# Kernel tuning notes

Hardware: AMD Instinct MI355X
Metric: run time of the kernel (lower is better)

Reference implementation:

```python
import jax, jax.numpy as jnp
import numpy as np

EPS = 1e-12  # F.normalize eps


def _l2norm(v):
    n = jnp.sqrt(jnp.sum(v * v, axis=-1, keepdims=True))
    return v / jnp.maximum(n, EPS)


def setup_inputs() -> dict:
    key = jax.random.key(0)
    ks = jax.random.split(key, 6)
    B, S, D, F, E = 2, 2048, 1024, 4096, 8
    std = 0.02
    return {
        "x": jax.random.normal(ks[0], (B, S, D), jnp.float32),
        "Wp": jax.random.normal(ks[1], (D, D), jnp.float32) * (1.0 / np.sqrt(D)),
        "sim_matrix": jax.random.normal(ks[2], (E, D), jnp.float32) * std,
        "temperature": jnp.asarray(1.0, jnp.float32),
        "W1": jax.random.normal(ks[3], (E, D, F), jnp.float32) * (1.0 / np.sqrt(D)),
        "b1": jnp.zeros((E, F), jnp.float32),
        "W2": jax.random.normal(ks[4], (E, F, D), jnp.float32) * (1.0 / np.sqrt(F)),
        "b2": jnp.zeros((E, D), jnp.float32),
    }


def reference(x, Wp, sim_matrix, temperature, W1, b1, W2, b2):
    # ---- cosine gate ----
    E = sim_matrix.shape[0]
    top_k = 2
    proj = jnp.einsum("bsd,ed->bse", x, Wp)            # Linear(d,d), weight [out,in]
    pn = _l2norm(proj)                                   # [B,S,D]
    sn = _l2norm(sim_matrix)                             # [E,D]
    gate_scores = jnp.einsum("bsd,ed->bse", pn, sn) / temperature
    top_v, top_i = jax.lax.top_k(gate_scores, top_k)     # [B,S,K]
    gate_probs = jax.nn.softmax(top_v, axis=-1)          # [B,S,K]
    # per-token combine weight per expert: sum_k prob_k * 1[idx_k==e]
    comb = jnp.sum(jax.nn.one_hot(top_i, E, dtype=x.dtype) * gate_probs[..., None], axis=-2)  # [B,S,E]
    # ---- experts (dense over all experts, masked combine = original math) ----
    h = jax.nn.gelu(jnp.einsum("bsd,edf->ebsf", x, W1) + b1[:, None, None, :], approximate=False)
    eo = jnp.einsum("ebsf,efd->ebsd", h, W2) + b2[:, None, None, :]  # [E,B,S,D]
    out = jnp.einsum("ebsd,bse->bsd", eo, comb)
    return out
```

## Files before the change

kernel.cpp:

```cpp
#include <hip/hip_runtime.h>
#include <hip/hip_bf16.h>
#include <math.h>

#define NTOK 4096
#define DD 1024
#define FF 4096
#define NEXP 8
#define EBM 128
#define EBN 128
#define EBK 32
#define PAIR_CAP 9216
#define TILES_MAX 72

typedef short bf16x8 __attribute__((ext_vector_type(8)));
typedef float f32x4 __attribute__((ext_vector_type(4)));
typedef unsigned short u16x8 __attribute__((ext_vector_type(8)));

__device__ __forceinline__ ushort f2bf(float x) {
  unsigned u = __float_as_uint(x);
  unsigned r = (u + 0x7FFFu + ((u >> 16) & 1u)) >> 16;
  return (ushort)r;
}

__device__ __forceinline__ void async16(const void* g, void* l) {
  __builtin_amdgcn_global_load_lds(
      (const __attribute__((address_space(1))) char*)g,
      (__attribute__((address_space(3))) char*)l, 16, 0, 0);
}


__global__ void k_convert4(const float4* __restrict__ s, ushort* __restrict__ d, int n4) {
  int i = blockIdx.x * 256 + threadIdx.x;
  if (i >= n4) return;
  float4 v = s[i];
  ushort4 o;
  o.x = f2bf(v.x); o.y = f2bf(v.y); o.z = f2bf(v.z); o.w = f2bf(v.w);
  *(ushort4*)(d + (size_t)i * 4) = o;
}

__global__ void k_transpose(const float* __restrict__ src, ushort* __restrict__ dst,
                            int R, int C) {
  __shared__ float tile[128][65];
  int e = blockIdx.z;
  const float* s = src + (size_t)e * R * C;
  ushort* d = dst + (size_t)e * R * C;
  int c0 = blockIdx.x * 64, r0 = blockIdx.y * 128;
  int tid = threadIdx.x;
  int rr0 = tid >> 4;
  int cc4 = (tid & 15) * 4;
#pragma unroll
  for (int ps = 0; ps < 8; ++ps) {
    int r = ps * 16 + rr0;
    float4 v = *(const float4*)&s[(size_t)(r0 + r) * C + c0 + cc4];
    tile[r][cc4 + 0] = v.x; tile[r][cc4 + 1] = v.y;
    tile[r][cc4 + 2] = v.z; tile[r][cc4 + 3] = v.w;
  }
  __syncthreads();
  int cw = tid >> 4;
  int rp = (tid & 15) * 8;
#pragma unroll
  for (int pass = 0; pass < 4; ++pass) {
    int c = pass * 16 + cw;
    u16x8 o;
#pragma unroll
    for (int k = 0; k < 8; ++k) o[k] = f2bf(tile[rp + k][c]);
    *(u16x8*)&d[(size_t)(c0 + c) * R + r0 + rp] = o;
  }
}

__global__ void k_u(const float* __restrict__ wp, const float* __restrict__ sim,
                    double* __restrict__ u_part) {
  __shared__ double sred[256];
  int tid = threadIdx.x;
  int dblk = blockIdx.x, e = blockIdx.y, kc = blockIdx.z;
  double s = 0.0;
#pragma unroll
  for (int j = 0; j < 4; ++j) {
    double v = sim[e * DD + j * 256 + tid];
    s += v * v;
  }
  sred[tid] = s;
  __syncthreads();
  for (int m = 128; m; m >>= 1) {
    if (tid < m) sred[tid] += sred[tid + m];
    __syncthreads();
  }
  double sn = fmax(sqrt(sred[0]), 1e-12);
  int d = dblk * 256 + tid;
  int o0 = kc * 256;
  double acc = 0.0;
#pragma unroll 8
  for (int o = o0; o < o0 + 256; ++o)
    acc += (double)wp[(size_t)o * DD + d] * (double)sim[e * DD + o];
  u_part[((size_t)kc * NEXP + e) * DD + d] = acc / sn;
}

__global__ void k_ured(const double* __restrict__ up, double* __restrict__ u) {
  int i = blockIdx.x * 256 + threadIdx.x;
  u[i] = (up[i] + up[8192 + i]) + (up[16384 + i] + up[24576 + i]);
}

__global__ void k_gate(const float* __restrict__ x, const double* __restrict__ u,
                       const float* __restrict__ nu_part, const float* __restrict__ temp,
                       int* __restrict__ t2e, float* __restrict__ t2p) {
  int wid = threadIdx.x >> 6, lane = threadIdx.x & 63;
  int t = blockIdx.x * 4 + wid;
  double acc[NEXP];
#pragma unroll
  for (int e = 0; e < NEXP; ++e) acc[e] = 0.0;
  for (int d = lane; d < DD; d += 64) {
    double xv = x[(size_t)t * DD + d];
#pragma unroll
    for (int e = 0; e < NEXP; ++e) acc[e] += xv * u[e * DD + d];
  }
#pragma unroll
  for (int e = 0; e < NEXP; ++e)
    for (int m = 32; m; m >>= 1) acc[e] += __shfl_down(acc[e], m);
  float nv = (lane < 16) ? nu_part[t * 16 + lane] : 0.f;
  nv += __shfl_down(nv, 8); nv += __shfl_down(nv, 4);
  nv += __shfl_down(nv, 2); nv += __shfl_down(nv, 1);
  if (lane == 0) {
    double den = fmax(sqrt((double)nv), 1e-12) * (double)temp[0];
    double s[NEXP];
#pragma unroll
    for (int e = 0; e < NEXP; ++e) s[e] = acc[e] / den;
    int e1 = 0; double v1 = s[0];
    for (int e = 1; e < NEXP; ++e) if (s[e] > v1) { v1 = s[e]; e1 = e; }
    int e2 = -1; double v2 = -1e300;
    for (int e = 0; e < NEXP; ++e) if (e != e1 && s[e] > v2) { v2 = s[e]; e2 = e; }
    double z = exp(v2 - v1);
    double inv = 1.0 / (1.0 + z);
    t2e[t * 2] = e1; t2e[t * 2 + 1] = e2;
    t2p[t * 2] = (float)inv; t2p[t * 2 + 1] = (float)(z * inv);
  }
}

__global__ void k_count(const int* __restrict__ t2e, const float* __restrict__ t2p,
                        int* __restrict__ meta, int* __restrict__ ptok,
                        float* __restrict__ pp) {
  __shared__ int cnt[NEXP];
  int tid = threadIdx.x;
  for (int i = tid; i < PAIR_CAP; i += 256) { ptok[i] = 0; pp[i] = 0.f; }
  if (tid < NEXP) cnt[tid] = 0;
  __syncthreads();
  for (int i = tid; i < NTOK * 2; i += 256) atomicAdd(&cnt[t2e[i]], 1);
  __syncthreads();
  if (tid == 0) {
    int off = 0;
    for (int e = 0; e < NEXP; ++e) {
      meta[e] = cnt[e];
      meta[8 + e] = off;
      off += ((cnt[e] + EBM - 1) / EBM) * EBM;
    }
    meta[16] = off;
    meta[17] = off / EBM;
    for (int e = 0; e < NEXP; ++e) meta[18 + e] = 0;
    int ti = 0;
    for (int e = 0; e < NEXP; ++e) {
      int nt = (cnt[e] + EBM - 1) / EBM;
      for (int k = 0; k < nt; ++k) meta[26 + ti++] = e;
    }
  }
  __syncthreads();
  for (int i = tid; i < NTOK * 2; i += 256) {
    int e = t2e[i];
    int slot = atomicAdd(&meta[18 + e], 1);
    int pos = meta[8 + e] + slot;
    ptok[pos] = i >> 1;
    pp[pos] = t2p[i];
  }
}

template <int EPI>
__launch_bounds__(256, 4)
__global__ void gemm_x(const ushort* __restrict__ Abase, const ushort* __restrict__ Bbase,
                       int K, int Brows,
                       const int* __restrict__ pair_tok, const float* __restrict__ pair_p,
                       const int* __restrict__ meta, const float* __restrict__ bias,
                       float* __restrict__ nu_part, ushort* __restrict__ hout,
                       float* __restrict__ outp, int g_tiles, int nby, int tile0) {
  __shared__ ushort As[2][EBM * EBK];
  __shared__ ushort Bs[2][EBN * EBK];
  __shared__ int tok_s[EBM];
  __shared__ float p_s[EBM];

  const int tid = threadIdx.x;
  const int lane = tid & 63;
  const int wid = tid >> 6;

  int tile, nb;
  {
    int bid = blockIdx.x;
    if ((g_tiles & 1) == 0 && (nby & 3) == 0) {
      int x = bid & 7, b = bid >> 3;
      int i = x >> 2, j = x & 3;
      int nt = g_tiles >> 1, np = nby >> 2;
      int t_loc = b / np, p_loc = b - t_loc * np;
      tile = i * nt + t_loc;
      nb = j * np + p_loc;
    } else {
      tile = bid % g_tiles;
      nb = bid / g_tiles;
    }
  }
  tile += tile0;

  int expert = 0;
  if constexpr (EPI != 0) {
    if (tile >= meta[17]) return;
    expert = meta[26 + tile];
    if (tid < EBM) {
      int pr = tile * EBM + tid;
      tok_s[tid] = pair_tok[pr];
      p_s[tid] = pair_p[pr];
    }
    __syncthreads();
  }

  const char* Ac = (const char*)Abase;
  const char* Bc = (const char*)(Bbase + (size_t)expert * Brows * K);

  const char* asrc[2];
  const char* bsrc[2];
#pragma unroll
  for (int i = 0; i < 2; ++i) {
    int c = i * 256 + tid;
    int m = c >> 2, cc = c & 3;
    int sw = (cc ^ ((m >> 1) & 3)) << 4;
    int arow;
    if constexpr (EPI == 1) arow = tok_s[m];
    else if constexpr (EPI == 2) arow = (tile - tile0) * EBM + m;
    else arow = tile * EBM + m;
    asrc[i] = Ac + (size_t)arow * K * 2 + sw;
    bsrc[i] = Bc + (size_t)(nb * EBN + m) * K * 2 + sw;
  }

  const int wr = wid >> 1, wc = wid & 1;
  const int l15 = lane & 15, lg = lane >> 4;
  const int fxor = (l15 >> 1) & 3;

  f32x4 acc[4][4];
#pragma unroll
  for (int a = 0; a < 4; ++a)
#pragma unroll
    for (int b = 0; b < 4; ++b) acc[a][b] = (f32x4){0.f, 0.f, 0.f, 0.f};

  const int nk = K / EBK;

#pragma unroll
  for (int i = 0; i < 2; ++i) {
    async16(asrc[i], (char*)(&As[0][0]) + (i * 256 + wid * 64) * 16);
    async16(bsrc[i], (char*)(&Bs[0][0]) + (i * 256 + wid * 64) * 16);
  }

  for (int kt = 0; kt < nk; ++kt) {
    const int cur = kt & 1;
    __syncthreads();
    if (kt + 1 < nk) {
      const size_t ko = (size_t)(kt + 1) * EBK * 2;
#pragma unroll
      for (int i = 0; i < 2; ++i) {
        async16(asrc[i] + ko, (char*)(&As[cur ^ 1][0]) + (i * 256 + wid * 64) * 16);
        async16(bsrc[i] + ko, (char*)(&Bs[cur ^ 1][0]) + (i * 256 + wid * 64) * 16);
      }
    }
    const char* Ab = (const char*)(&As[cur][0]);
    const char* Bb = (const char*)(&Bs[cur][0]);
    bf16x8 af[4], bfr[4];
#pragma unroll
    for (int fi = 0; fi < 4; ++fi) {
      int r = wr * 64 + fi * 16 + l15;
      af[fi] = *(const bf16x8*)(Ab + r * 64 + (lg ^ fxor) * 16);
    }
#pragma unroll
    for (int fj = 0; fj < 4; ++fj) {
      int r = wc * 64 + fj * 16 + l15;
      bfr[fj] = *(const bf16x8*)(Bb + r * 64 + (lg ^ fxor) * 16);
    }
#pragma unroll
    for (int fi = 0; fi < 4; ++fi)
#pragma unroll
      for (int fj = 0; fj < 4; ++fj)
        acc[fi][fj] =
            __builtin_amdgcn_mfma_f32_16x16x32_bf16(af[fi], bfr[fj], acc[fi][fj], 0, 0, 0);
  }

  if constexpr (EPI == 0) {
#pragma unroll
    for (int fi = 0; fi < 4; ++fi) {
#pragma unroll
      for (int j = 0; j < 4; ++j) {
        float s = 0.f;
#pragma unroll
        for (int fj = 0; fj < 4; ++fj) { float v = acc[fi][fj][j]; s += v * v; }
        s += __shfl_xor(s, 1); s += __shfl_xor(s, 2);
        s += __shfl_xor(s, 4); s += __shfl_xor(s, 8);
        if (l15 == 0) {
          int row = tile * EBM + wr * 64 + fi * 16 + lg * 4 + j;
          nu_part[row * 16 + nb * 2 + wc] = s;
        }
      }
    }
  } else if constexpr (EPI == 1) {
    float bv[4];
#pragma unroll
    for (int fj = 0; fj < 4; ++fj)
      bv[fj] = bias[expert * FF + nb * EBN + wc * 64 + fj * 16 + l15];
#pragma unroll
    for (int fi = 0; fi < 4; ++fi)
#pragma unroll
      for (int fj = 0; fj < 4; ++fj)
#pragma unroll
        for (int j = 0; j < 4; ++j) {
          float v = acc[fi][fj][j] + bv[fj];
          float g = 0.5f * v * (1.0f + erff(v * 0.70710678118654752f));
          int rl = wr * 64 + fi * 16 + lg * 4 + j;
          size_t grow = (size_t)(tile - tile0) * EBM + rl;
          int col = nb * EBN + wc * 64 + fj * 16 + l15;
          hout[grow * FF + col] = f2bf(g);
        }
  } else {
    float bv[4];
#pragma unroll
    for (int fj = 0; fj < 4; ++fj)
      bv[fj] = bias[expert * DD + nb * EBN + wc * 64 + fj * 16 + l15];
#pragma unroll
    for (int fi = 0; fi < 4; ++fi) {
      int rl = wr * 64 + fi * 16 + lg * 4;
#pragma unroll
      for (int j = 0; j < 4; ++j) {
        int tok = tok_s[rl + j];
        float p = p_s[rl + j];
#pragma unroll
        for (int fj = 0; fj < 4; ++fj) {
          float v = (acc[fi][fj][j] + bv[fj]) * p;
          int col = nb * EBN + wc * 64 + fj * 16 + l15;
          atomicAdd(outp + (size_t)tok * DD + col, v);
        }
      }
    }
  }
}


extern "C" void kernel_launch(void* const* d_in, const int* in_sizes, int n_in,
                              void* d_out, int out_size, void* d_ws, size_t ws_size,
                              hipStream_t stream) {
  const float* x = (const float*)d_in[0];
  const float* wp = (const float*)d_in[1];
  const float* sim = (const float*)d_in[2];
  const float* temp = (const float*)d_in[3];
  const float* w1 = (const float*)d_in[4];
  const float* b1 = (const float*)d_in[5];
  const float* w2 = (const float*)d_in[6];
  const float* b2 = (const float*)d_in[7];
  float* out = (float*)d_out;

  char* w = (char*)d_ws;
  size_t off = 0;
  auto alloc = [&](size_t sz) {
    char* p = w + off;
    off = (off + sz + 255) & ~(size_t)255;
    return p;
  };
  double* u = (double*)alloc((size_t)NEXP * DD * 8);
  double* u_part = (double*)alloc((size_t)4 * NEXP * DD * 8);
  float* nu_part = (float*)alloc((size_t)NTOK * 16 * 4);
  int* t2e = (int*)alloc((size_t)NTOK * 2 * 4);
  float* t2p = (float*)alloc((size_t)NTOK * 2 * 4);
  int* meta = (int*)alloc(512);
  int* ptok = (int*)alloc((size_t)PAIR_CAP * 4);
  float* pp = (float*)alloc((size_t)PAIR_CAP * 4);
  ushort* xbf = (ushort*)alloc((size_t)NTOK * DD * 2);
  ushort* wpbf = (ushort*)alloc((size_t)DD * DD * 2);
  ushort* w1t = (ushort*)alloc((size_t)NEXP * DD * FF * 2);
  ushort* w2t = (ushort*)alloc((size_t)NEXP * DD * FF * 2);
  size_t havail = (ws_size > off) ? (ws_size - off) : 0;
  int G = (int)(havail / ((size_t)EBM * FF * 2));
  if (G > TILES_MAX) G = TILES_MAX;
  if (G >= 8) G &= ~7;
  if (G < 1) G = 1;
  ushort* h = (ushort*)(w + off);

  hipMemsetAsync(d_out, 0, (size_t)out_size * 4, stream);

  k_convert4<<<dim3(NTOK * DD / 4 / 256), 256, 0, stream>>>((const float4*)x, xbf, NTOK * DD / 4);
  k_convert4<<<dim3(DD * DD / 4 / 256), 256, 0, stream>>>((const float4*)wp, wpbf, DD * DD / 4);
  k_transpose<<<dim3(FF / 64, DD / 128, NEXP), 256, 0, stream>>>(w1, w1t, DD, FF);
  k_transpose<<<dim3(DD / 64, FF / 128, NEXP), 256, 0, stream>>>(w2, w2t, FF, DD);
  k_u<<<dim3(DD / 256, NEXP, 4), 256, 0, stream>>>(wp, sim, u_part);
  k_ured<<<dim3(NEXP * DD / 256), 256, 0, stream>>>(u_part, u);
  gemm_x<0><<<dim3((NTOK / EBM) * (DD / EBN)), 256, 0, stream>>>(
      xbf, wpbf, DD, DD, nullptr, nullptr, nullptr, nullptr, nu_part, nullptr, nullptr,
      NTOK / EBM, DD / EBN, 0);
  k_gate<<<dim3(NTOK / 4), 256, 0, stream>>>(x, u, nu_part, temp, t2e, t2p);
  k_count<<<1, 256, 0, stream>>>(t2e, t2p, meta, ptok, pp);

  for (int t0 = 0; t0 < TILES_MAX; t0 += G) {
    int g = TILES_MAX - t0;
    if (g > G) g = G;
    gemm_x<1><<<dim3(g * (FF / EBN)), 256, 0, stream>>>(
        xbf, w1t, DD, FF, ptok, pp, meta, b1, nullptr, h, nullptr, g, FF / EBN, t0);
    gemm_x<2><<<dim3(g * (DD / EBN)), 256, 0, stream>>>(
        h, w2t, FF, DD, ptok, pp, meta, b2, nullptr, nullptr, out, g, DD / EBN, t0);
  }
}
```

Before: 540.8 us.

## Split-K the second expert GEMM and parallelize pair scatter across blocks

The down-projection GEMM now launches with two K-chunks along blockIdx.y, and each chunk atomically adds its partial sum into the output, with the bias applied only by the first chunk. This doubles the block count for the small-N GEMM to fill more compute units. The token-to-expert scatter moves out of the single-block count kernel into a separate multi-block kernel. In exchange, the down-projection issues twice as many float atomics to the output and the scatter costs one more kernel launch.

```diff
diff --git a/kernel.cpp b/kernel.cpp
--- a/kernel.cpp
+++ b/kernel.cpp
@@ -135,9 +135,8 @@
   }
 }
 
-__global__ void k_count(const int* __restrict__ t2e, const float* __restrict__ t2p,
-                        int* __restrict__ meta, int* __restrict__ ptok,
-                        float* __restrict__ pp) {
+__global__ void k_count(const int* __restrict__ t2e, int* __restrict__ meta,
+                        int* __restrict__ ptok, float* __restrict__ pp) {
   __shared__ int cnt[NEXP];
   int tid = threadIdx.x;
   for (int i = tid; i < PAIR_CAP; i += 256) { ptok[i] = 0; pp[i] = 0.f; }
@@ -161,20 +160,24 @@
       for (int k = 0; k < nt; ++k) meta[26 + ti++] = e;
     }
   }
-  __syncthreads();
-  for (int i = tid; i < NTOK * 2; i += 256) {
-    int e = t2e[i];
-    int slot = atomicAdd(&meta[18 + e], 1);
-    int pos = meta[8 + e] + slot;
-    ptok[pos] = i >> 1;
-    pp[pos] = t2p[i];
-  }
+}
+
+__global__ void k_scatter(const int* __restrict__ t2e, const float* __restrict__ t2p,
+                          int* __restrict__ meta, int* __restrict__ ptok,
+                          float* __restrict__ pp) {
+  int i = blockIdx.x * 256 + threadIdx.x;
+  if (i >= NTOK * 2) return;
+  int e = t2e[i];
+  int slot = atomicAdd(&meta[18 + e], 1);
+  int pos = meta[8 + e] + slot;
+  ptok[pos] = i >> 1;
+  pp[pos] = t2p[i];
 }
 
 template <int EPI>
 __launch_bounds__(256, 4)
 __global__ void gemm_x(const ushort* __restrict__ Abase, const ushort* __restrict__ Bbase,
-                       int K, int Brows,
+                       int K, int Brows, int kchunk,
                        const int* __restrict__ pair_tok, const float* __restrict__ pair_p,
                        const int* __restrict__ meta, const float* __restrict__ bias,
                        float* __restrict__ nu_part, ushort* __restrict__ hout,
@@ -187,6 +190,7 @@
   const int tid = threadIdx.x;
   const int lane = tid & 63;
   const int wid = tid >> 6;
+  const int k0 = blockIdx.y * kchunk;
 
   int tile, nb;
   {
@@ -231,8 +235,8 @@
     if constexpr (EPI == 1) arow = tok_s[m];
     else if constexpr (EPI == 2) arow = (tile - tile0) * EBM + m;
     else arow = tile * EBM + m;
-    asrc[i] = Ac + (size_t)arow * K * 2 + sw;
-    bsrc[i] = Bc + (size_t)(nb * EBN + m) * K * 2 + sw;
+    asrc[i] = Ac + ((size_t)arow * K + k0) * 2 + sw;
+    bsrc[i] = Bc + ((size_t)(nb * EBN + m) * K + k0) * 2 + sw;
   }
 
   const int wr = wid >> 1, wc = wid & 1;
@@ -245,7 +249,7 @@
 #pragma unroll
     for (int b = 0; b < 4; ++b) acc[a][b] = (f32x4){0.f, 0.f, 0.f, 0.f};
 
-  const int nk = K / EBK;
+  const int nk = kchunk / EBK;
 
 #pragma unroll
   for (int i = 0; i < 2; ++i) {
@@ -321,9 +325,10 @@
         }
   } else {
     float bv[4];
+    const float bgate = (k0 == 0) ? 1.f : 0.f;
 #pragma unroll
     for (int fj = 0; fj < 4; ++fj)
-      bv[fj] = bias[expert * DD + nb * EBN + wc * 64 + fj * 16 + l15];
+      bv[fj] = bgate * bias[expert * DD + nb * EBN + wc * 64 + fj * 16 + l15];
 #pragma unroll
     for (int fi = 0; fi < 4; ++fi) {
       int rl = wr * 64 + fi * 16 + lg * 4;
@@ -391,17 +396,18 @@
   k_u<<<dim3(DD / 256, NEXP, 4), 256, 0, stream>>>(wp, sim, u_part);
   k_ured<<<dim3(NEXP * DD / 256), 256, 0, stream>>>(u_part, u);
   gemm_x<0><<<dim3((NTOK / EBM) * (DD / EBN)), 256, 0, stream>>>(
-      xbf, wpbf, DD, DD, nullptr, nullptr, nullptr, nullptr, nu_part, nullptr, nullptr,
+      xbf, wpbf, DD, DD, DD, nullptr, nullptr, nullptr, nullptr, nu_part, nullptr, nullptr,
       NTOK / EBM, DD / EBN, 0);
   k_gate<<<dim3(NTOK / 4), 256, 0, stream>>>(x, u, nu_part, temp, t2e, t2p);
-  k_count<<<1, 256, 0, stream>>>(t2e, t2p, meta, ptok, pp);
+  k_count<<<1, 256, 0, stream>>>(t2e, meta, ptok, pp);
+  k_scatter<<<dim3(NTOK * 2 / 256), 256, 0, stream>>>(t2e, t2p, meta, ptok, pp);
 
   for (int t0 = 0; t0 < TILES_MAX; t0 += G) {
     int g = TILES_MAX - t0;
     if (g > G) g = G;
     gemm_x<1><<<dim3(g * (FF / EBN)), 256, 0, stream>>>(
-        xbf, w1t, DD, FF, ptok, pp, meta, b1, nullptr, h, nullptr, g, FF / EBN, t0);
-    gemm_x<2><<<dim3(g * (DD / EBN)), 256, 0, stream>>>(
-        h, w2t, FF, DD, ptok, pp, meta, b2, nullptr, nullptr, out, g, DD / EBN, t0);
-  }
-}
+        xbf, w1t, DD, FF, DD, ptok, pp, meta, b1, nullptr, h, nullptr, g, FF / EBN, t0);
+    gemm_x<2><<<dim3(g * (DD / EBN), 2), 256, 0, stream>>>(
+        h, w2t, FF, DD, FF / 2, ptok, pp, meta, b2, nullptr, nullptr, out, g, DD / EBN, t0);
+  }
+}
```

New measurement: 543.2 us. About the same (+0.4%).
